# Performance work log

Hardware: AMD Instinct MI355X
Metric: run time of the kernel (lower is better)

The kernel has to match this reference:

```python
import jax, jax.numpy as jnp
import numpy as np

_SIZE = 9  # kernel half-width -> 19x19 kernel
_EPS = 0.0001

def _gaussian_kernel(size: int, mean: float, std: float) -> jnp.ndarray:
    t = jnp.arange(-size, size + 1, dtype=jnp.float32)
    # Normal(mean, std) pdf
    vals = jnp.exp(-0.5 * ((t - mean) / std) ** 2) / (std * np.sqrt(2.0 * np.pi))
    k2d = jnp.outer(vals, vals)
    return k2d / jnp.sum(k2d)

def _blur(x, k):
    # x: [B,H,W,3], k: [19,19]; depthwise conv, SAME padding, same kernel per channel
    kern = jnp.tile(k[:, :, None, None], (1, 1, 1, 3))  # HWIO with I=1, O=3 (grouped)
    return jax.lax.conv_general_dilated(
        x, kern, window_strides=(1, 1), padding='SAME',
        dimension_numbers=('NHWC', 'HWIO', 'NHWC'), feature_group_count=3)

def setup_inputs() -> dict:
    key = jax.random.key(0)
    k1, k2 = jax.random.split(key)
    x0 = jax.random.uniform(k1, (32, 512, 512, 3), dtype=jnp.float32)
    mask = jnp.ones((32, 512, 512, 1), dtype=jnp.float32)
    return {"x0": x0, "mask": mask}

def reference(x0, mask):
    k = _gaussian_kernel(_SIZE, 0.0, 1.0)
    mean = _blur(x0, k)                      # local mean per channel
    centered = x0 - mean
    var = _blur(centered ** 2, k)            # local variance per channel
    std = jnp.sqrt(var) + _EPS
    out = (centered / std) * mask            # mask broadcasts over channel dim
    # Original concatenates in order [red, blue, green] where split gives
    # channels (0,1,2) named (red, blue, green) -> output channel order == input order.
    return out
```

## Files before the change

### kernel.cpp

```cpp
#include <hip/hip_runtime.h>
#include <math.h>


#define TW 32
#define TH 32
#define S1W 132
#define S1R 52
#define B2R 42

__global__ __launch_bounds__(256, 3)
void lecun_lcn_kernel(const float* __restrict__ x,
                      const float* __restrict__ mask,
                      float* __restrict__ out)
{
    __shared__ float s1[S1R * S1W];
    __shared__ float b2[B2R * S1W];

    const int tid = threadIdx.x;
    const int w0  = blockIdx.x * TW;
    const int h0  = blockIdx.y * TH;
    const int bi  = blockIdx.z;
    const int fc0 = 3 * w0 - 15;

    const float K[6] = {
        3.9894227826685783e-01f,
        2.4197072322439816e-01f,
        5.3990966224238430e-02f,
        4.4318483882270000e-03f,
        1.3383022504889000e-04f,
        1.4867195067806000e-06f
    };

    const float* xb = x + (size_t)bi * 512 * 1536;

    for (int t = tid; t < S1R * 8; t += 256) {
        const int r   = t >> 3;
        const int run = t & 7;
        const int h   = h0 - 10 + r;
        float* dst = &s1[r * S1W + run * 16];
        if ((unsigned)h >= 512u) {
            float4 z = make_float4(0.f, 0.f, 0.f, 0.f);
            ((float4*)dst)[0] = z; ((float4*)dst)[1] = z;
            ((float4*)dst)[2] = z; ((float4*)dst)[3] = z;
            continue;
        }
        const float* xrow = xb + (size_t)h * 1536;
        const int gc0 = fc0 + run * 16;
        const int a   = gc0 - 17;
        float w[48];
        if (a >= 0 && a <= 1536 - 48) {
            const float4* p = (const float4*)(xrow + a);
            #pragma unroll
            for (int q = 0; q < 12; ++q) {
                float4 v = p[q];
                w[4*q+0] = v.x; w[4*q+1] = v.y; w[4*q+2] = v.z; w[4*q+3] = v.w;
            }
        } else {
            #pragma unroll
            for (int i = 0; i < 48; ++i) {
                int j = a + i;
                w[i] = ((unsigned)j < 1536u) ? xrow[j] : 0.0f;
            }
        }
        float v1[16];
        #pragma unroll
        for (int i = 0; i < 16; ++i) {
            const int ci = 17 + i;
            float acc = K[0] * w[ci];
            #pragma unroll
            for (int d = 1; d <= 5; ++d)
                acc = fmaf(K[d], w[ci - 3*d] + w[ci + 3*d], acc);
            v1[i] = acc;
        }
        ((float4*)dst)[0] = make_float4(v1[0],  v1[1],  v1[2],  v1[3]);
        ((float4*)dst)[1] = make_float4(v1[4],  v1[5],  v1[6],  v1[7]);
        ((float4*)dst)[2] = make_float4(v1[8],  v1[9],  v1[10], v1[11]);
        ((float4*)dst)[3] = make_float4(v1[12], v1[13], v1[14], v1[15]);
    }
    __syncthreads();

    {
        const int quad = tid & 31;
        const int rt   = tid >> 5;
        const int cnt  = (rt < 6) ? 5 : 6;
        const int rb   = (rt < 6) ? 5 * rt : 30 + 6 * (rt - 6);
        const int c4   = quad * 4;
        const int gcb  = fc0 + c4;
        const bool cv0 = (unsigned)(gcb + 0) < 1536u;
        const bool cv1 = (unsigned)(gcb + 1) < 1536u;
        const bool cv2 = (unsigned)(gcb + 2) < 1536u;
        const bool cv3 = (unsigned)(gcb + 3) < 1536u;
        float4 w[16];
        #pragma unroll
        for (int k = 0; k < 16; ++k) {
            if (k < cnt + 10)
                w[k] = *(const float4*)&s1[(rb + k) * S1W + c4];
        }
        #pragma unroll
        for (int j = 0; j < 6; ++j) {
            if (j < cnt) {
                const int r = rb + j;
                const int h = h0 - 5 + r;
                float4* dst = (float4*)&b2[r * S1W + c4];
                if ((unsigned)h >= 512u) {
                    *dst = make_float4(0.f, 0.f, 0.f, 0.f);
                } else {
                    float m0 = K[0] * w[j+5].x, m1 = K[0] * w[j+5].y;
                    float m2 = K[0] * w[j+5].z, m3 = K[0] * w[j+5].w;
                    #pragma unroll
                    for (int d = 1; d <= 5; ++d) {
                        float4 aa = w[j + 5 - d];
                        float4 bb = w[j + 5 + d];
                        m0 = fmaf(K[d], aa.x + bb.x, m0);
                        m1 = fmaf(K[d], aa.y + bb.y, m1);
                        m2 = fmaf(K[d], aa.z + bb.z, m2);
                        m3 = fmaf(K[d], aa.w + bb.w, m3);
                    }
                    const float* xrow = xb + (size_t)h * 1536;
                    float c0 = cv0 ? (xrow[gcb + 0] - m0) : 0.0f;
                    float c1 = cv1 ? (xrow[gcb + 1] - m1) : 0.0f;
                    float c2 = cv2 ? (xrow[gcb + 2] - m2) : 0.0f;
                    float c3 = cv3 ? (xrow[gcb + 3] - m3) : 0.0f;
                    *dst = make_float4(c0, c1, c2, c3);
                }
            }
        }
    }
    __syncthreads();

    float* vc = s1;
    {
        const int quad = tid & 31;
        const int rt   = tid >> 5;
        const int r0   = rt * 4;
        const int c4   = quad * 4;
        float4 w[14];
        #pragma unroll
        for (int k = 0; k < 14; ++k) {
            float4 v = *(const float4*)&b2[(r0 + k) * S1W + c4];
            w[k] = make_float4(v.x*v.x, v.y*v.y, v.z*v.z, v.w*v.w);
        }
        #pragma unroll
        for (int j = 0; j < 4; ++j) {
            float s0 = K[0] * w[j+5].x, s1v = K[0] * w[j+5].y;
            float s2v = K[0] * w[j+5].z, s3 = K[0] * w[j+5].w;
            #pragma unroll
            for (int d = 1; d <= 5; ++d) {
                float4 aa = w[j + 5 - d];
                float4 bb = w[j + 5 + d];
                s0  = fmaf(K[d], aa.x + bb.x, s0);
                s1v = fmaf(K[d], aa.y + bb.y, s1v);
                s2v = fmaf(K[d], aa.z + bb.z, s2v);
                s3  = fmaf(K[d], aa.w + bb.w, s3);
            }
            *(float4*)&vc[(r0 + j) * S1W + c4] = make_float4(s0, s1v, s2v, s3);
        }
    }
    __syncthreads();

    {
        const int r    = tid >> 3;
        const int run  = tid & 7;
        const int tc0  = run * 12;
        float w[44];
        #pragma unroll
        for (int q = 0; q < 11; ++q) {
            float4 v = *(const float4*)&vc[r * S1W + tc0 + 4*q];
            w[4*q+0] = v.x; w[4*q+1] = v.y; w[4*q+2] = v.z; w[4*q+3] = v.w;
        }
        float cw[16];
        #pragma unroll
        for (int q = 0; q < 4; ++q) {
            float4 v = *(const float4*)&b2[(r + 5) * S1W + tc0 + 12 + 4*q];
            cw[4*q+0] = v.x; cw[4*q+1] = v.y; cw[4*q+2] = v.z; cw[4*q+3] = v.w;
        }
        const int h = h0 + r;
        const size_t rowoff = (size_t)(bi * 512 + h);
        const float* mrow = mask + rowoff * 512 + w0 + 4 * run;
        float mv[4];
        #pragma unroll
        for (int k = 0; k < 4; ++k) mv[k] = mrow[k];
        float o[12];
        #pragma unroll
        for (int j = 0; j < 12; ++j) {
            const int ci = 15 + j;
            float var = K[0] * w[ci];
            #pragma unroll
            for (int d = 1; d <= 5; ++d)
                var = fmaf(K[d], w[ci - 3*d] + w[ci + 3*d], var);
            o[j] = cw[j + 3] * __builtin_amdgcn_rcpf(sqrtf(var) + 1e-4f) * mv[j / 3];
        }
        float* orow = &out[rowoff * 1536 + 3 * w0 + tc0];
        ((float4*)orow)[0] = make_float4(o[0], o[1], o[2],  o[3]);
        ((float4*)orow)[1] = make_float4(o[4], o[5], o[6],  o[7]);
        ((float4*)orow)[2] = make_float4(o[8], o[9], o[10], o[11]);
    }
}

extern "C" void kernel_launch(void* const* d_in, const int* in_sizes, int n_in,
                              void* d_out, int out_size, void* d_ws, size_t ws_size,
                              hipStream_t stream) {
    const float* x0   = (const float*)d_in[0];
    const float* mask = (const float*)d_in[1];
    float* out = (float*)d_out;

    dim3 grid(512 / TW, 512 / TH, 32);
    dim3 block(256);
    lecun_lcn_kernel<<<grid, block, 0, stream>>>(x0, mask, out);
}
```

Before: 309.3 us.

## Use ring buffer for first-pass blur rows to cut LDS and raise occupancy

Shrinks the horizontal-blur shared buffer from 52 rows to a 32-row ring. The mean/centering stage is now done in two halves, with the second batch of horizontally blurred rows written into ring slots the first half has finished with. Less LDS per block allows launch bounds to request 4 blocks per CU instead of 3, hiding memory latency better. The cost is two extra block-wide barriers, more serialized phases, and an uneven second phase where only 160 of 256 threads load.

```diff
diff --git a/kernel.cpp b/kernel.cpp
--- a/kernel.cpp
+++ b/kernel.cpp
@@ -5,15 +5,15 @@
 #define TW 32
 #define TH 32
 #define S1W 132
-#define S1R 52
+#define RING 32
 #define B2R 42
 
-__global__ __launch_bounds__(256, 3)
+__global__ __launch_bounds__(256, 4)
 void lecun_lcn_kernel(const float* __restrict__ x,
                       const float* __restrict__ mask,
                       float* __restrict__ out)
 {
-    __shared__ float s1[S1R * S1W];
+    __shared__ float s1h[RING * S1W];
     __shared__ float b2[B2R * S1W];
 
     const int tid = threadIdx.x;
@@ -33,71 +33,71 @@
 
     const float* xb = x + (size_t)bi * 512 * 1536;
 
-    for (int t = tid; t < S1R * 8; t += 256) {
-        const int r   = t >> 3;
-        const int run = t & 7;
+    {
+        const int r   = tid >> 3;
+        const int run = tid & 7;
         const int h   = h0 - 10 + r;
-        float* dst = &s1[r * S1W + run * 16];
+        float* dst = &s1h[r * S1W + run * 16];
         if ((unsigned)h >= 512u) {
             float4 z = make_float4(0.f, 0.f, 0.f, 0.f);
             ((float4*)dst)[0] = z; ((float4*)dst)[1] = z;
             ((float4*)dst)[2] = z; ((float4*)dst)[3] = z;
-            continue;
-        }
-        const float* xrow = xb + (size_t)h * 1536;
-        const int gc0 = fc0 + run * 16;
-        const int a   = gc0 - 17;
-        float w[48];
-        if (a >= 0 && a <= 1536 - 48) {
-            const float4* p = (const float4*)(xrow + a);
+        } else {
+            const float* xrow = xb + (size_t)h * 1536;
+            const int gc0 = fc0 + run * 16;
+            const int a   = gc0 - 17;
+            float w[48];
+            if (a >= 0 && a <= 1536 - 48) {
+                const float4* p = (const float4*)(xrow + a);
+                #pragma unroll
+                for (int q = 0; q < 12; ++q) {
+                    float4 v = p[q];
+                    w[4*q+0] = v.x; w[4*q+1] = v.y; w[4*q+2] = v.z; w[4*q+3] = v.w;
+                }
+            } else {
+                #pragma unroll
+                for (int i = 0; i < 48; ++i) {
+                    int j = a + i;
+                    w[i] = ((unsigned)j < 1536u) ? xrow[j] : 0.0f;
+                }
+            }
+            float v1[16];
             #pragma unroll
-            for (int q = 0; q < 12; ++q) {
-                float4 v = p[q];
-                w[4*q+0] = v.x; w[4*q+1] = v.y; w[4*q+2] = v.z; w[4*q+3] = v.w;
-            }
-        } else {
-            #pragma unroll
-            for (int i = 0; i < 48; ++i) {
-                int j = a + i;
-                w[i] = ((unsigned)j < 1536u) ? xrow[j] : 0.0f;
-            }
-        }
-        float v1[16];
-        #pragma unroll
-        for (int i = 0; i < 16; ++i) {
-            const int ci = 17 + i;
-            float acc = K[0] * w[ci];
-            #pragma unroll
-            for (int d = 1; d <= 5; ++d)
-                acc = fmaf(K[d], w[ci - 3*d] + w[ci + 3*d], acc);
-            v1[i] = acc;
-        }
-        ((float4*)dst)[0] = make_float4(v1[0],  v1[1],  v1[2],  v1[3]);
-        ((float4*)dst)[1] = make_float4(v1[4],  v1[5],  v1[6],  v1[7]);
-        ((float4*)dst)[2] = make_float4(v1[8],  v1[9],  v1[10], v1[11]);
-        ((float4*)dst)[3] = make_float4(v1[12], v1[13], v1[14], v1[15]);
+            for (int i = 0; i < 16; ++i) {
+                const int ci = 17 + i;
+                float acc = K[0] * w[ci];
+                #pragma unroll
+                for (int d = 1; d <= 5; ++d)
+                    acc = fmaf(K[d], w[ci - 3*d] + w[ci + 3*d], acc);
+                v1[i] = acc;
+            }
+            ((float4*)dst)[0] = make_float4(v1[0],  v1[1],  v1[2],  v1[3]);
+            ((float4*)dst)[1] = make_float4(v1[4],  v1[5],  v1[6],  v1[7]);
+            ((float4*)dst)[2] = make_float4(v1[8],  v1[9],  v1[10], v1[11]);
+            ((float4*)dst)[3] = make_float4(v1[12], v1[13], v1[14], v1[15]);
+        }
     }
     __syncthreads();
 
     {
         const int quad = tid & 31;
         const int rt   = tid >> 5;
-        const int cnt  = (rt < 6) ? 5 : 6;
-        const int rb   = (rt < 6) ? 5 * rt : 30 + 6 * (rt - 6);
+        const int cnt  = (rt < 6) ? 3 : 2;
+        const int rb   = (rt < 6) ? 3 * rt : 18 + 2 * (rt - 6);
         const int c4   = quad * 4;
         const int gcb  = fc0 + c4;
         const bool cv0 = (unsigned)(gcb + 0) < 1536u;
         const bool cv1 = (unsigned)(gcb + 1) < 1536u;
         const bool cv2 = (unsigned)(gcb + 2) < 1536u;
         const bool cv3 = (unsigned)(gcb + 3) < 1536u;
-        float4 w[16];
-        #pragma unroll
-        for (int k = 0; k < 16; ++k) {
+        float4 w[13];
+        #pragma unroll
+        for (int k = 0; k < 13; ++k) {
             if (k < cnt + 10)
-                w[k] = *(const float4*)&s1[(rb + k) * S1W + c4];
-        }
-        #pragma unroll
-        for (int j = 0; j < 6; ++j) {
+                w[k] = *(const float4*)&s1h[(rb + k) * S1W + c4];
+        }
+        #pragma unroll
+        for (int j = 0; j < 3; ++j) {
             if (j < cnt) {
                 const int r = rb + j;
                 const int h = h0 - 5 + r;
@@ -128,7 +128,102 @@
     }
     __syncthreads();
 
-    float* vc = s1;
+    if (tid < 20 * 8) {
+        const int r2  = tid >> 3;
+        const int run = tid & 7;
+        const int h   = h0 + 22 + r2;
+        float* dst = &s1h[r2 * S1W + run * 16];
+        if ((unsigned)h >= 512u) {
+            float4 z = make_float4(0.f, 0.f, 0.f, 0.f);
+            ((float4*)dst)[0] = z; ((float4*)dst)[1] = z;
+            ((float4*)dst)[2] = z; ((float4*)dst)[3] = z;
+        } else {
+            const float* xrow = xb + (size_t)h * 1536;
+            const int gc0 = fc0 + run * 16;
+            const int a   = gc0 - 17;
+            float w[48];
+            if (a >= 0 && a <= 1536 - 48) {
+                const float4* p = (const float4*)(xrow + a);
+                #pragma unroll
+                for (int q = 0; q < 12; ++q) {
+                    float4 v = p[q];
+                    w[4*q+0] = v.x; w[4*q+1] = v.y; w[4*q+2] = v.z; w[4*q+3] = v.w;
+                }
+            } else {
+                #pragma unroll
+                for (int i = 0; i < 48; ++i) {
+                    int j = a + i;
+                    w[i] = ((unsigned)j < 1536u) ? xrow[j] : 0.0f;
+                }
+            }
+            float v1[16];
+            #pragma unroll
+            for (int i = 0; i < 16; ++i) {
+                const int ci = 17 + i;
+                float acc = K[0] * w[ci];
+                #pragma unroll
+                for (int d = 1; d <= 5; ++d)
+                    acc = fmaf(K[d], w[ci - 3*d] + w[ci + 3*d], acc);
+                v1[i] = acc;
+            }
+            ((float4*)dst)[0] = make_float4(v1[0],  v1[1],  v1[2],  v1[3]);
+            ((float4*)dst)[1] = make_float4(v1[4],  v1[5],  v1[6],  v1[7]);
+            ((float4*)dst)[2] = make_float4(v1[8],  v1[9],  v1[10], v1[11]);
+            ((float4*)dst)[3] = make_float4(v1[12], v1[13], v1[14], v1[15]);
+        }
+    }
+    __syncthreads();
+
+    {
+        const int quad = tid & 31;
+        const int rt   = tid >> 5;
+        const int cnt  = (rt < 4) ? 3 : 2;
+        const int rb   = (rt < 4) ? 22 + 3 * rt : 34 + 2 * (rt - 4);
+        const int c4   = quad * 4;
+        const int gcb  = fc0 + c4;
+        const bool cv0 = (unsigned)(gcb + 0) < 1536u;
+        const bool cv1 = (unsigned)(gcb + 1) < 1536u;
+        const bool cv2 = (unsigned)(gcb + 2) < 1536u;
+        const bool cv3 = (unsigned)(gcb + 3) < 1536u;
+        float4 w[13];
+        #pragma unroll
+        for (int k = 0; k < 13; ++k) {
+            if (k < cnt + 10)
+                w[k] = *(const float4*)&s1h[((rb + k) & 31) * S1W + c4];
+        }
+        #pragma unroll
+        for (int j = 0; j < 3; ++j) {
+            if (j < cnt) {
+                const int r = rb + j;
+                const int h = h0 - 5 + r;
+                float4* dst = (float4*)&b2[r * S1W + c4];
+                if ((unsigned)h >= 512u) {
+                    *dst = make_float4(0.f, 0.f, 0.f, 0.f);
+                } else {
+                    float m0 = K[0] * w[j+5].x, m1 = K[0] * w[j+5].y;
+                    float m2 = K[0] * w[j+5].z, m3 = K[0] * w[j+5].w;
+                    #pragma unroll
+                    for (int d = 1; d <= 5; ++d) {
+                        float4 aa = w[j + 5 - d];
+                        float4 bb = w[j + 5 + d];
+                        m0 = fmaf(K[d], aa.x + bb.x, m0);
+                        m1 = fmaf(K[d], aa.y + bb.y, m1);
+                        m2 = fmaf(K[d], aa.z + bb.z, m2);
+                        m3 = fmaf(K[d], aa.w + bb.w, m3);
+                    }
+                    const float* xrow = xb + (size_t)h * 1536;
+                    float c0 = cv0 ? (xrow[gcb + 0] - m0) : 0.0f;
+                    float c1 = cv1 ? (xrow[gcb + 1] - m1) : 0.0f;
+                    float c2 = cv2 ? (xrow[gcb + 2] - m2) : 0.0f;
+                    float c3 = cv3 ? (xrow[gcb + 3] - m3) : 0.0f;
+                    *dst = make_float4(c0, c1, c2, c3);
+                }
+            }
+        }
+    }
+    __syncthreads();
+
+    float* vc = s1h;
     {
         const int quad = tid & 31;
         const int rt   = tid >> 5;
```

Result: no change. 307.0 us (-0.8%).

## Double tile height to 64 rows with ring-buffered shared staging and 512 threads

Applied to the files above, without the earlier changes.

Tiles grow to 32x64 output pixels per block with 512 threads. Shared memory is kept small by running the horizontal pass in two phases over a 48-row ring buffer, and the variance and output passes in two halves. The goal is to cut the halo overhead of the separable 11-tap blurs, which recompute 20 extra rows per 32-row tile. In exchange the kernel needs more __syncthreads barriers, leaves some threads idle in several phases (for example, only 256 of 512 threads run the output pass), and may run at lower occupancy.

```diff
diff --git a/kernel.cpp b/kernel.cpp
--- a/kernel.cpp
+++ b/kernel.cpp
@@ -3,17 +3,18 @@
 
 
 #define TW 32
-#define TH 32
+#define TH 64
 #define S1W 132
-#define S1R 52
-#define B2R 42
-
-__global__ __launch_bounds__(256, 3)
+#define S1R 48
+#define B2R 74
+#define NT  512
+
+__global__ __launch_bounds__(NT, 4)
 void lecun_lcn_kernel(const float* __restrict__ x,
                       const float* __restrict__ mask,
                       float* __restrict__ out)
 {
-    __shared__ float s1[S1R * S1W];
+    __shared__ float s1h[S1R * S1W];
     __shared__ float b2[B2R * S1W];
 
     const int tid = threadIdx.x;
@@ -33,16 +34,14 @@
 
     const float* xb = x + (size_t)bi * 512 * 1536;
 
-    for (int t = tid; t < S1R * 8; t += 256) {
-        const int r   = t >> 3;
-        const int run = t & 7;
-        const int h   = h0 - 10 + r;
-        float* dst = &s1[r * S1W + run * 16];
+    auto p1_task = [&](int ss, int slot, int run) {
+        const int h = h0 - 10 + ss;
+        float* dst = &s1h[slot * S1W + run * 16];
         if ((unsigned)h >= 512u) {
             float4 z = make_float4(0.f, 0.f, 0.f, 0.f);
             ((float4*)dst)[0] = z; ((float4*)dst)[1] = z;
             ((float4*)dst)[2] = z; ((float4*)dst)[3] = z;
-            continue;
+            return;
         }
         const float* xrow = xb + (size_t)h * 1536;
         const int gc0 = fc0 + run * 16;
@@ -76,32 +75,31 @@
         ((float4*)dst)[1] = make_float4(v1[4],  v1[5],  v1[6],  v1[7]);
         ((float4*)dst)[2] = make_float4(v1[8],  v1[9],  v1[10], v1[11]);
         ((float4*)dst)[3] = make_float4(v1[12], v1[13], v1[14], v1[15]);
-    }
-    __syncthreads();
-
-    {
+    };
+
+    auto p2_run = [&](int rb, int cnt) {
         const int quad = tid & 31;
-        const int rt   = tid >> 5;
-        const int cnt  = (rt < 6) ? 5 : 6;
-        const int rb   = (rt < 6) ? 5 * rt : 30 + 6 * (rt - 6);
         const int c4   = quad * 4;
         const int gcb  = fc0 + c4;
         const bool cv0 = (unsigned)(gcb + 0) < 1536u;
         const bool cv1 = (unsigned)(gcb + 1) < 1536u;
         const bool cv2 = (unsigned)(gcb + 2) < 1536u;
         const bool cv3 = (unsigned)(gcb + 3) < 1536u;
-        float4 w[16];
-        #pragma unroll
-        for (int k = 0; k < 16; ++k) {
-            if (k < cnt + 10)
-                w[k] = *(const float4*)&s1[(rb + k) * S1W + c4];
-        }
-        #pragma unroll
-        for (int j = 0; j < 6; ++j) {
+        float4 w[13];
+        #pragma unroll
+        for (int k = 0; k < 13; ++k) {
+            if (k < cnt + 10) {
+                const int ss = rb + k;
+                const int sl = (ss >= S1R) ? ss - S1R : ss;
+                w[k] = *(const float4*)&s1h[sl * S1W + c4];
+            }
+        }
+        #pragma unroll
+        for (int j = 0; j < 3; ++j) {
             if (j < cnt) {
-                const int r = rb + j;
-                const int h = h0 - 5 + r;
-                float4* dst = (float4*)&b2[r * S1W + c4];
+                const int br = rb + j;
+                const int h = h0 - 5 + br;
+                float4* dst = (float4*)&b2[br * S1W + c4];
                 if ((unsigned)h >= 512u) {
                     *dst = make_float4(0.f, 0.f, 0.f, 0.f);
                 } else {
@@ -125,23 +123,22 @@
                 }
             }
         }
-    }
-    __syncthreads();
-
-    float* vc = s1;
-    {
+    };
+
+    float* vc = s1h;
+    auto p3_half = [&](int vbase) {
         const int quad = tid & 31;
         const int rt   = tid >> 5;
-        const int r0   = rt * 4;
         const int c4   = quad * 4;
-        float4 w[14];
-        #pragma unroll
-        for (int k = 0; k < 14; ++k) {
-            float4 v = *(const float4*)&b2[(r0 + k) * S1W + c4];
-            w[k] = make_float4(v.x*v.x, v.y*v.y, v.z*v.z, v.w*v.w);
-        }
-        #pragma unroll
-        for (int j = 0; j < 4; ++j) {
+        const int v0   = vbase + 2 * rt;
+        float4 w[12];
+        #pragma unroll
+        for (int k = 0; k < 12; ++k) {
+            float4 t = *(const float4*)&b2[(v0 + k) * S1W + c4];
+            w[k] = make_float4(t.x*t.x, t.y*t.y, t.z*t.z, t.w*t.w);
+        }
+        #pragma unroll
+        for (int j = 0; j < 2; ++j) {
             float s0 = K[0] * w[j+5].x, s1v = K[0] * w[j+5].y;
             float s2v = K[0] * w[j+5].z, s3 = K[0] * w[j+5].w;
             #pragma unroll
@@ -153,19 +150,20 @@
                 s2v = fmaf(K[d], aa.z + bb.z, s2v);
                 s3  = fmaf(K[d], aa.w + bb.w, s3);
             }
-            *(float4*)&vc[(r0 + j) * S1W + c4] = make_float4(s0, s1v, s2v, s3);
-        }
-    }
-    __syncthreads();
-
-    {
-        const int r    = tid >> 3;
+            *(float4*)&vc[(v0 - vbase + j) * S1W + c4] =
+                make_float4(s0, s1v, s2v, s3);
+        }
+    };
+
+    auto p4_half = [&](int rbase) {
+        if (tid >= 256) return;
+        const int r    = rbase + (tid >> 3);
         const int run  = tid & 7;
         const int tc0  = run * 12;
         float w[44];
         #pragma unroll
         for (int q = 0; q < 11; ++q) {
-            float4 v = *(const float4*)&vc[r * S1W + tc0 + 4*q];
+            float4 v = *(const float4*)&vc[(r - rbase) * S1W + tc0 + 4*q];
             w[4*q+0] = v.x; w[4*q+1] = v.y; w[4*q+2] = v.z; w[4*q+3] = v.w;
         }
         float cw[16];
@@ -194,7 +192,37 @@
         ((float4*)orow)[0] = make_float4(o[0], o[1], o[2],  o[3]);
         ((float4*)orow)[1] = make_float4(o[4], o[5], o[6],  o[7]);
         ((float4*)orow)[2] = make_float4(o[8], o[9], o[10], o[11]);
+    };
+
+    if (tid < 384) p1_task(tid >> 3, tid >> 3, tid & 7);
+    __syncthreads();
+
+    {
+        const int rt  = tid >> 5;
+        const int cnt = (rt < 6) ? 3 : 2;
+        const int rb  = (rt < 6) ? 3 * rt : 18 + 2 * (rt - 6);
+        p2_run(rb, cnt);
     }
+    __syncthreads();
+
+    if (tid < 288) p1_task(48 + (tid >> 3), tid >> 3, tid & 7);
+    __syncthreads();
+
+    {
+        const int rt  = tid >> 5;
+        const int cnt = (rt < 4) ? 3 : 2;
+        const int rb  = (rt < 4) ? 38 + 3 * rt : 50 + 2 * (rt - 4);
+        p2_run(rb, cnt);
+    }
+    __syncthreads();
+
+    p3_half(0);
+    __syncthreads();
+    p4_half(0);
+    __syncthreads();
+    p3_half(32);
+    __syncthreads();
+    p4_half(32);
 }
 
 extern "C" void kernel_launch(void* const* d_in, const int* in_sizes, int n_in,
@@ -205,6 +233,6 @@
     float* out = (float*)d_out;
 
     dim3 grid(512 / TW, 512 / TH, 32);
-    dim3 block(256);
+    dim3 block(NT);
     lecun_lcn_kernel<<<grid, block, 0, stream>>>(x0, mask, out);
 }
```

After: 309.9 us. Within noise of the previous version (+0.2%).
